# Optimization experiments

Hardware: AMD Instinct MI355X
Metric: run time of the kernel (lower is better)

Reference implementation:

```python
import jax, jax.numpy as jnp
import numpy as np

E = 1024
H = 16
F = 4096
EPS = 1e-5


def layer_norm(x, gamma, beta):
    mu = jnp.mean(x, axis=-1, keepdims=True)
    var = jnp.var(x, axis=-1, keepdims=True)
    return (x - mu) * jax.lax.rsqrt(var + EPS) * gamma + beta


def setup_inputs() -> dict:
    key = jax.random.key(0)
    ks = jax.random.split(key, 12)
    s = lambda d: 1.0 / np.sqrt(d)
    x = jax.random.normal(ks[0], (2, 2048, E), dtype=jnp.float32)
    Wq = jax.random.uniform(ks[1], (E, E), minval=-s(E), maxval=s(E))
    bq = jnp.zeros((E,), jnp.float32)
    Wk = jax.random.uniform(ks[2], (E, E), minval=-s(E), maxval=s(E))
    bk = jnp.zeros((E,), jnp.float32)
    Wv = jax.random.uniform(ks[3], (E, E), minval=-s(E), maxval=s(E))
    bv = jnp.zeros((E,), jnp.float32)
    Wo = jax.random.uniform(ks[4], (E, E), minval=-s(E), maxval=s(E))
    bo = jnp.zeros((E,), jnp.float32)
    g1 = jnp.ones((E,), jnp.float32)
    b1 = jnp.zeros((E,), jnp.float32)
    W1 = jax.random.uniform(ks[5], (E, F), minval=-s(E), maxval=s(E))
    bf1 = jnp.zeros((F,), jnp.float32)
    W2 = jax.random.uniform(ks[6], (F, E), minval=-s(F), maxval=s(F))
    bf2 = jnp.zeros((E,), jnp.float32)
    g2 = jnp.ones((E,), jnp.float32)
    b2 = jnp.zeros((E,), jnp.float32)
    return dict(x=x, Wq=Wq, bq=bq, Wk=Wk, bk=bk, Wv=Wv, bv=bv, Wo=Wo, bo=bo,
                g1=g1, b1=b1, W1=W1, bf1=bf1, W2=W2, bf2=bf2, g2=g2, b2=b2)


def reference(x, Wq, bq, Wk, bk, Wv, bv, Wo, bo, g1, b1, W1, bf1, W2, bf2, g2, b2):
    B, L, _ = x.shape
    Dh = E // H
    q = (x @ Wq + bq).reshape(B, L, H, Dh).transpose(0, 2, 1, 3)  # b h l d
    k = (x @ Wk + bk).reshape(B, L, H, Dh).transpose(0, 2, 1, 3)  # computed but unused (faithful to source)
    v = (x @ Wv + bv).reshape(B, L, H, Dh).transpose(0, 2, 1, 3)
    # NOTE: source computes scores as Q @ V^T (not K), scaled, then softmax
    scores = jnp.einsum('bhqd,bhkd->bhqk', q, v) / jnp.sqrt(jnp.float32(Dh))
    att = jax.nn.softmax(scores, axis=-1)
    ctx = jnp.einsum('bhqk,bhkd->bhqd', att, v)
    ctx = ctx.transpose(0, 2, 1, 3).reshape(B, L, E)
    att_out = ctx @ Wo + bo
    post_att = layer_norm(x + att_out, g1, b1)
    ff = jax.nn.relu(post_att @ W1 + bf1) @ W2 + bf2
    return layer_norm(post_att + ff, g2, b2)
```

## Files before the change

### kernel.cpp

```cpp
#include <hip/hip_runtime.h>
#include <stdint.h>

typedef unsigned short u16;
typedef __attribute__((ext_vector_type(8))) short short8;
typedef __attribute__((ext_vector_type(4))) float f32x4;
typedef __attribute__((ext_vector_type(4))) unsigned short u16x4;

#define TOKENS 4096
#define E_DIM 1024
#define F_DIM 4096
#define SEQ 2048
#define NH 16
#define DH 64

__device__ __forceinline__ u16 f2b(float f) {
  union { float f; unsigned u; } v; v.f = f;
  unsigned r = v.u + 0x7fffu + ((v.u >> 16) & 1u);
  return (u16)(r >> 16);
}

__device__ __forceinline__ void gl2lds16(const u16* g, u16* l) {
  __builtin_amdgcn_global_load_lds(
      (const __attribute__((address_space(1))) unsigned int*)(size_t)(g),
      (__attribute__((address_space(3))) unsigned int*)(unsigned int)(size_t)(l),
      16, 0, 0);
}

__global__ __launch_bounds__(256)
void transpose_w(const float* __restrict__ W, u16* __restrict__ Wt, int K, int N) {
  __shared__ float tile[32][33];
  const int kb = blockIdx.x * 32, nb = blockIdx.y * 32;
  const int tx = threadIdx.x & 31, ty = threadIdx.x >> 5;
#pragma unroll
  for (int i = 0; i < 32; i += 8)
    tile[ty + i][tx] = W[(size_t)(kb + ty + i) * N + nb + tx];
  __syncthreads();
#pragma unroll
  for (int i = 0; i < 32; i += 8)
    Wt[(size_t)(nb + ty + i) * K + kb + tx] = f2b(tile[tx][ty + i]);
}

__global__ __launch_bounds__(256)
void f32_to_bf16(const float* __restrict__ in, u16* __restrict__ out) {
  const int i = blockIdx.x * 256 + threadIdx.x;
  f32x4 f = ((const f32x4*)in)[i];
  u16x4 u;
#pragma unroll
  for (int j = 0; j < 4; j++) u[j] = f2b(f[j]);
  ((u16x4*)out)[i] = u;
}

__global__ __launch_bounds__(256)
void transpose_v(const u16* __restrict__ vsrc, u16* __restrict__ vt) {
  __shared__ u16 tile[32][66];
  const int kb = blockIdx.x * 32;
  const int bh = blockIdx.y;
  const int b = bh >> 4, h = bh & 15;
  {
    const int tx = threadIdx.x & 63, ty = threadIdx.x >> 6;
#pragma unroll
    for (int i = 0; i < 32; i += 4)
      tile[ty + i][tx] = vsrc[(size_t)(b * SEQ + kb + ty + i) * E_DIM + h * DH + tx];
  }
  __syncthreads();
  {
    const int kk = threadIdx.x & 31, dd = threadIdx.x >> 5;
#pragma unroll
    for (int j = 0; j < 64; j += 8)
      vt[(size_t)(bh * DH + dd + j) * SEQ + kb + kk] = tile[kk][dd + j];
  }
}

template <int RELU, int OUTBF>
__global__ __launch_bounds__(256)
void gemm_bt(const u16* __restrict__ A, const u16* __restrict__ Bt,
             const float* __restrict__ bias, void* __restrict__ Cout,
             int M, int N, int K) {
  __shared__ __align__(16) u16 As[128 * 32];
  __shared__ __align__(16) u16 Bs[128 * 32];
  const int tid = threadIdx.x;
  const int lane = tid & 63, wave = tid >> 6;
  const int mBlk = blockIdx.y * 128, nBlk = blockIdx.x * 128;
  const int wm = (wave >> 1) * 64, wn = (wave & 1) * 64;
  const int l15 = lane & 15, g = lane >> 4;

  f32x4 acc[4][4] = {};

  const int srow = lane >> 2;
  const int scol = (lane & 3) * 8;

  const u16* Ab = A + (size_t)mBlk * K;
  const u16* Bb = Bt + (size_t)nBlk * K;

  for (int k0 = 0; k0 < K; k0 += 32) {
    __syncthreads();
    for (int c = wave; c < 8; c += 4) {
      const int r = c * 16 + srow;
      gl2lds16(Ab + (size_t)r * K + k0 + scol, As + c * 512 + lane * 8);
      gl2lds16(Bb + (size_t)r * K + k0 + scol, Bs + c * 512 + lane * 8);
    }
    __syncthreads();

    short8 af[4], bf[4];
#pragma unroll
    for (int i = 0; i < 4; i++)
      af[i] = *(const short8*)(As + (wm + i * 16 + l15) * 32 + g * 8);
#pragma unroll
    for (int i = 0; i < 4; i++)
      bf[i] = *(const short8*)(Bs + (wn + i * 16 + l15) * 32 + g * 8);
#pragma unroll
    for (int mi = 0; mi < 4; mi++)
#pragma unroll
      for (int ni = 0; ni < 4; ni++)
        acc[mi][ni] = __builtin_amdgcn_mfma_f32_16x16x32_bf16(af[mi], bf[ni],
                                                              acc[mi][ni], 0, 0, 0);
  }

  const int row0 = mBlk + wm + g * 4;
  const int col0 = nBlk + wn + l15;
#pragma unroll
  for (int ni = 0; ni < 4; ni++) {
    const int c = col0 + ni * 16;
    const float bv = bias[c];
#pragma unroll
    for (int mi = 0; mi < 4; mi++) {
#pragma unroll
      for (int r = 0; r < 4; r++) {
        float v = acc[mi][ni][r] + bv;
        if (RELU) v = fmaxf(v, 0.f);
        const size_t idx = (size_t)(row0 + mi * 16 + r) * N + c;
        if (OUTBF) ((u16*)Cout)[idx] = f2b(v);
        else       ((float*)Cout)[idx] = v;
      }
    }
  }
}

template <int RELU, int OUTBF>
__global__ __launch_bounds__(256)
void gemm_bt64(const u16* __restrict__ A, const u16* __restrict__ Bt,
               const float* __restrict__ bias, void* __restrict__ Cout,
               int M, int N, int K, float oscale) {
  __shared__ __align__(16) u16 As[128 * 32];
  __shared__ __align__(16) u16 Bs[64 * 32];
  const int tid = threadIdx.x;
  const int lane = tid & 63, wave = tid >> 6;
  const int mBlk = blockIdx.y * 128, nBlk = blockIdx.x * 64;
  const int wm = (wave >> 1) * 64, wn = (wave & 1) * 32;
  const int l15 = lane & 15, g = lane >> 4;

  f32x4 acc[4][2] = {};

  const int srow = lane >> 2;
  const int scol = (lane & 3) * 8;

  const u16* Ab = A + (size_t)mBlk * K;
  const u16* Bb = Bt + (size_t)nBlk * K;

  for (int k0 = 0; k0 < K; k0 += 32) {
    __syncthreads();
    for (int c = wave; c < 8; c += 4) {
      const int r = c * 16 + srow;
      gl2lds16(Ab + (size_t)r * K + k0 + scol, As + c * 512 + lane * 8);
    }
    gl2lds16(Bb + (size_t)(wave * 16 + srow) * K + k0 + scol, Bs + wave * 512 + lane * 8);
    __syncthreads();

    short8 af[4], bf[2];
#pragma unroll
    for (int i = 0; i < 4; i++)
      af[i] = *(const short8*)(As + (wm + i * 16 + l15) * 32 + g * 8);
#pragma unroll
    for (int i = 0; i < 2; i++)
      bf[i] = *(const short8*)(Bs + (wn + i * 16 + l15) * 32 + g * 8);
#pragma unroll
    for (int mi = 0; mi < 4; mi++)
#pragma unroll
      for (int ni = 0; ni < 2; ni++)
        acc[mi][ni] = __builtin_amdgcn_mfma_f32_16x16x32_bf16(af[mi], bf[ni],
                                                              acc[mi][ni], 0, 0, 0);
  }

  const int row0 = mBlk + wm + g * 4;
  const int col0 = nBlk + wn + l15;
#pragma unroll
  for (int ni = 0; ni < 2; ni++) {
    const int c = col0 + ni * 16;
    const float bv = bias[c];
#pragma unroll
    for (int mi = 0; mi < 4; mi++) {
#pragma unroll
      for (int r = 0; r < 4; r++) {
        float v = (acc[mi][ni][r] + bv) * oscale;
        if (RELU) v = fmaxf(v, 0.f);
        const size_t idx = (size_t)(row0 + mi * 16 + r) * N + c;
        if (OUTBF) ((u16*)Cout)[idx] = f2b(v);
        else       ((float*)Cout)[idx] = v;
      }
    }
  }
}

__global__ __launch_bounds__(256)
void gemm_qv64(const u16* __restrict__ A, const u16* __restrict__ Bqv,
               const float* __restrict__ bq, const float* __restrict__ bv,
               u16* __restrict__ qout, u16* __restrict__ vout, int K) {
  __shared__ __align__(16) u16 As[128 * 32];
  __shared__ __align__(16) u16 Bs[64 * 32];
  const int tid = threadIdx.x;
  const int lane = tid & 63, wave = tid >> 6;
  const int mBlk = blockIdx.y * 128, nBlk = blockIdx.x * 64;
  const int isQ = nBlk < 1024;
  const int ncol = isQ ? nBlk : nBlk - 1024;
  const float* bias = isQ ? bq : bv;
  u16* out = isQ ? qout : vout;
  const float oscale = isQ ? 0.125f : 1.0f;
  const int wm = (wave >> 1) * 64, wn = (wave & 1) * 32;
  const int l15 = lane & 15, g = lane >> 4;

  f32x4 acc[4][2] = {};

  const int srow = lane >> 2;
  const int scol = (lane & 3) * 8;

  const u16* Ab = A + (size_t)mBlk * K;
  const u16* Bb = Bqv + (size_t)nBlk * K;

  for (int k0 = 0; k0 < K; k0 += 32) {
    __syncthreads();
    for (int c = wave; c < 8; c += 4) {
      const int r = c * 16 + srow;
      gl2lds16(Ab + (size_t)r * K + k0 + scol, As + c * 512 + lane * 8);
    }
    gl2lds16(Bb + (size_t)(wave * 16 + srow) * K + k0 + scol, Bs + wave * 512 + lane * 8);
    __syncthreads();

    short8 af[4], bf[2];
#pragma unroll
    for (int i = 0; i < 4; i++)
      af[i] = *(const short8*)(As + (wm + i * 16 + l15) * 32 + g * 8);
#pragma unroll
    for (int i = 0; i < 2; i++)
      bf[i] = *(const short8*)(Bs + (wn + i * 16 + l15) * 32 + g * 8);
#pragma unroll
    for (int mi = 0; mi < 4; mi++)
#pragma unroll
      for (int ni = 0; ni < 2; ni++)
        acc[mi][ni] = __builtin_amdgcn_mfma_f32_16x16x32_bf16(af[mi], bf[ni],
                                                              acc[mi][ni], 0, 0, 0);
  }

  const int row0 = mBlk + wm + g * 4;
  const int col0 = ncol + wn + l15;
#pragma unroll
  for (int ni = 0; ni < 2; ni++) {
    const int c = col0 + ni * 16;
    const float bv_ = bias[c];
#pragma unroll
    for (int mi = 0; mi < 4; mi++) {
#pragma unroll
      for (int r = 0; r < 4; r++) {
        float v = (acc[mi][ni][r] + bv_) * oscale;
        out[(size_t)(row0 + mi * 16 + r) * E_DIM + c] = f2b(v);
      }
    }
  }
}

__global__ __launch_bounds__(256)
void attn_kernel(const u16* __restrict__ qb, const u16* __restrict__ vb,
                 const u16* __restrict__ vtb, u16* __restrict__ ctxb) {
  __shared__ __align__(16) u16 Vs[64 * 64];
  __shared__ __align__(16) u16 Vts[64 * 64];
  __shared__ __align__(16) u16 Pl[4][16 * 64];
  const int tid = threadIdx.x;
  const int lane = tid & 63;
  const int wave = tid >> 6;
  const int l15 = lane & 15;
  const int g = lane >> 4;
  const int qblk = blockIdx.x;
  const int bh = blockIdx.y;
  const int b = bh >> 4;
  const int h = bh & 15;
  const int qrow = qblk * 64 + wave * 16;

  short8 aq0, aq1;
  {
    const u16* qp = qb + ((size_t)(b * SEQ + qrow + l15)) * E_DIM + h * DH + g * 8;
    aq0 = *(const short8*)(qp);
    aq1 = *(const short8*)(qp + 32);
  }

  f32x4 o[4] = {};
  float lsum[4] = {0.f, 0.f, 0.f, 0.f};

  const u16* vbase = vb + ((size_t)b * SEQ) * E_DIM + h * DH;
  const u16* vtbase = vtb + ((size_t)bh * DH) * SEQ;
  u16* myPl = Pl[wave];

  const int srow = tid >> 3;
  const int sch = tid & 7;

  for (int kc = 0; kc < SEQ; kc += 64) {
    __syncthreads();
#pragma unroll
    for (int j = 0; j < 2; j++) {
      const int key = j * 32 + srow;
      gl2lds16(vbase + (size_t)(kc + key) * E_DIM + ((sch ^ (key & 7)) * 8),
               Vs + key * 64 + sch * 8);
      const int d = j * 32 + srow;
      gl2lds16(vtbase + (size_t)d * SEQ + kc + ((sch ^ (d & 7)) * 8),
               Vts + d * 64 + sch * 8);
    }
    __syncthreads();

    f32x4 s[4];
#pragma unroll
    for (int nt = 0; nt < 4; nt++) {
      const int key = nt * 16 + l15;
      const u16* vr = Vs + key * 64;
      short8 b0 = *(const short8*)(vr + ((g ^ (key & 7)) * 8));
      short8 b1 = *(const short8*)(vr + (((4 + g) ^ (key & 7)) * 8));
      f32x4 z = {};
      z = __builtin_amdgcn_mfma_f32_16x16x32_bf16(aq0, b0, z, 0, 0, 0);
      z = __builtin_amdgcn_mfma_f32_16x16x32_bf16(aq1, b1, z, 0, 0, 0);
      s[nt] = z;
    }

#pragma unroll
    for (int r = 0; r < 4; r++) {
      const int q = g * 4 + r;
      u16* prow = myPl + q * 64;
#pragma unroll
      for (int nt = 0; nt < 4; nt++) {
        union { float f; unsigned u; } pv;
        pv.f = __expf(s[nt][r]);
        union { unsigned u; float f; } pt;
        pt.u = pv.u & 0xffff0000u;
        lsum[r] += pt.f;
        prow[(((nt * 2 + (l15 >> 3)) ^ (q & 7)) * 8) + (l15 & 7)] = (u16)(pt.u >> 16);
      }
    }

#pragma unroll
    for (int ks = 0; ks < 2; ks++) {
      short8 ap = *(const short8*)(myPl + l15 * 64 + (((ks * 4 + g) ^ (l15 & 7)) * 8));
#pragma unroll
      for (int dt = 0; dt < 4; dt++) {
        const int d = dt * 16 + l15;
        short8 bv = *(const short8*)(Vts + d * 64 + (((ks * 4 + g) ^ (d & 7)) * 8));
        o[dt] = __builtin_amdgcn_mfma_f32_16x16x32_bf16(ap, bv, o[dt], 0, 0, 0);
      }
    }
  }

#pragma unroll
  for (int r = 0; r < 4; r++) {
    float l = lsum[r];
    l += __shfl_xor(l, 1);
    l += __shfl_xor(l, 2);
    l += __shfl_xor(l, 4);
    l += __shfl_xor(l, 8);
    const float inv = 1.0f / l;
    size_t base = ((size_t)(b * SEQ + qrow + g * 4 + r)) * E_DIM + h * DH;
#pragma unroll
    for (int dt = 0; dt < 4; dt++)
      ctxb[base + dt * 16 + l15] = f2b(o[dt][r] * inv);
  }
}

__global__ __launch_bounds__(256)
void add_ln(const float* __restrict__ X, const float* __restrict__ Y,
            const float* __restrict__ gam, const float* __restrict__ bet,
            float* __restrict__ out32, u16* __restrict__ out16) {
  const int row = blockIdx.x;
  const int tid = threadIdx.x;
  const size_t base = (size_t)row * E_DIM;
  float v[4];
  float s = 0.f, sq = 0.f;
#pragma unroll
  for (int i = 0; i < 4; i++) {
    const int c = tid + i * 256;
    float x = X[base + c] + Y[base + c];
    v[i] = x; s += x; sq += x * x;
  }
#pragma unroll
  for (int off = 32; off; off >>= 1) {
    s += __shfl_xor(s, off);
    sq += __shfl_xor(sq, off);
  }
  __shared__ float sh[8];
  const int wave = tid >> 6, lane = tid & 63;
  if (lane == 0) { sh[wave] = s; sh[4 + wave] = sq; }
  __syncthreads();
  s = sh[0] + sh[1] + sh[2] + sh[3];
  sq = sh[4] + sh[5] + sh[6] + sh[7];
  const float mean = s * (1.f / 1024.f);
  const float var = sq * (1.f / 1024.f) - mean * mean;
  const float rstd = rsqrtf(var + 1e-5f);
#pragma unroll
  for (int i = 0; i < 4; i++) {
    const int c = tid + i * 256;
    float y = (v[i] - mean) * rstd * gam[c] + bet[c];
    out32[base + c] = y;
    if (out16) out16[base + c] = f2b(y);
  }
}

extern "C" void kernel_launch(void* const* d_in, const int* in_sizes, int n_in,
                              void* d_out, int out_size, void* d_ws, size_t ws_size,
                              hipStream_t stream) {
  const float* x   = (const float*)d_in[0];
  const float* Wq  = (const float*)d_in[1];
  const float* bq  = (const float*)d_in[2];
  const float* Wv  = (const float*)d_in[5];
  const float* bv  = (const float*)d_in[6];
  const float* Wo  = (const float*)d_in[7];
  const float* bo  = (const float*)d_in[8];
  const float* g1  = (const float*)d_in[9];
  const float* b1  = (const float*)d_in[10];
  const float* W1  = (const float*)d_in[11];
  const float* bf1 = (const float*)d_in[12];
  const float* W2  = (const float*)d_in[13];
  const float* bf2 = (const float*)d_in[14];
  const float* g2  = (const float*)d_in[15];
  const float* b2  = (const float*)d_in[16];

  char* w = (char*)d_ws;
  const size_t MB = 1024ull * 1024ull;
  u16*   xb   = (u16*)(w + 0);
  u16*   h1   = (u16*)(w + 8 * MB);
  u16*   qb   = (u16*)(w + 8 * MB);
  u16*   vb   = (u16*)(w + 16 * MB);
  u16*   vtb  = (u16*)(w + 24 * MB);
  u16*   ctxb = (u16*)(w + 32 * MB);
  float* atto = (float*)(w + 40 * MB);
  float* ff   = (float*)(w + 40 * MB);
  float* pa   = (float*)(w + 56 * MB);
  u16*   pab  = (u16*)(w + 72 * MB);
  u16*   WqT  = (u16*)(w + 80 * MB);
  u16*   WvT  = (u16*)(w + 82 * MB);
  u16*   WoT  = (u16*)(w + 84 * MB);
  u16*   W1T  = (u16*)(w + 86 * MB);
  u16*   W2T  = (u16*)(w + 94 * MB);

  transpose_w<<<dim3(32, 32), 256, 0, stream>>>(Wq, WqT, 1024, 1024);
  transpose_w<<<dim3(32, 32), 256, 0, stream>>>(Wv, WvT, 1024, 1024);
  transpose_w<<<dim3(32, 32), 256, 0, stream>>>(Wo, WoT, 1024, 1024);
  transpose_w<<<dim3(32, 128), 256, 0, stream>>>(W1, W1T, 1024, 4096);
  transpose_w<<<dim3(128, 32), 256, 0, stream>>>(W2, W2T, 4096, 1024);
  f32_to_bf16<<<TOKENS * E_DIM / 4 / 256, 256, 0, stream>>>(x, xb);

  gemm_qv64<<<dim3(32, 32), 256, 0, stream>>>(xb, WqT, bq, bv, qb, vb, 1024);
  transpose_v<<<dim3(64, 32), 256, 0, stream>>>(vb, vtb);
  attn_kernel<<<dim3(32, 32), 256, 0, stream>>>(qb, vb, vtb, ctxb);
  gemm_bt64<0, 0><<<dim3(16, 32), 256, 0, stream>>>(ctxb, WoT, bo, atto, TOKENS, 1024, 1024, 1.0f);
  add_ln<<<TOKENS, 256, 0, stream>>>(x, atto, g1, b1, pa, pab);
  gemm_bt<1, 1><<<dim3(32, 32), 256, 0, stream>>>(pab, W1T, bf1, h1, TOKENS, 4096, 1024);
  gemm_bt64<0, 0><<<dim3(16, 32), 256, 0, stream>>>(h1, W2T, bf2, ff, TOKENS, 1024, 4096, 1.0f);
  add_ln<<<TOKENS, 256, 0, stream>>>(pa, ff, g2, b2, (float*)d_out, (u16*)nullptr);
}
```

Before: 409.0 us.

## Use split-K 128x128 GEMM for N=1024 projections, reduce partials in add-LN

Replaces the 128x64-tile GEMM for the Wo and W2 projections with a 128x128-tile kernel that splits K into two halves over blockIdx.z. Each half writes its own fp32 partial buffer, with the bias added only by the first half. The layernorm kernel now sums both partials with the residual, so the reduction is fused there. The larger tile gives more data reuse per block and split-K keeps the block count at 512. The cost is extra fp32 traffic from writing and reading a second 16MB partial buffer, and the workspace layout is shifted to make room for it.

```diff
diff --git a/kernel.cpp b/kernel.cpp
--- a/kernel.cpp
+++ b/kernel.cpp
@@ -85,7 +85,6 @@
   const int l15 = lane & 15, g = lane >> 4;
 
   f32x4 acc[4][4] = {};
-
   const int srow = lane >> 2;
   const int scol = (lane & 3) * 8;
 
@@ -136,67 +135,63 @@
   }
 }
 
-template <int RELU, int OUTBF>
-__global__ __launch_bounds__(256)
-void gemm_bt64(const u16* __restrict__ A, const u16* __restrict__ Bt,
-               const float* __restrict__ bias, void* __restrict__ Cout,
-               int M, int N, int K, float oscale) {
+__global__ __launch_bounds__(256)
+void gemm_bt_sk(const u16* __restrict__ A, const u16* __restrict__ Bt,
+                const float* __restrict__ bias, float* __restrict__ Cout,
+                int M, int N, int K) {
   __shared__ __align__(16) u16 As[128 * 32];
-  __shared__ __align__(16) u16 Bs[64 * 32];
+  __shared__ __align__(16) u16 Bs[128 * 32];
   const int tid = threadIdx.x;
   const int lane = tid & 63, wave = tid >> 6;
-  const int mBlk = blockIdx.y * 128, nBlk = blockIdx.x * 64;
-  const int wm = (wave >> 1) * 64, wn = (wave & 1) * 32;
+  const int mBlk = blockIdx.y * 128, nBlk = blockIdx.x * 128;
+  const int kz = blockIdx.z;
+  const int Kh = K >> 1;
+  const int wm = (wave >> 1) * 64, wn = (wave & 1) * 64;
   const int l15 = lane & 15, g = lane >> 4;
 
-  f32x4 acc[4][2] = {};
-
+  f32x4 acc[4][4] = {};
   const int srow = lane >> 2;
   const int scol = (lane & 3) * 8;
 
-  const u16* Ab = A + (size_t)mBlk * K;
-  const u16* Bb = Bt + (size_t)nBlk * K;
-
-  for (int k0 = 0; k0 < K; k0 += 32) {
+  const u16* Ab = A + (size_t)mBlk * K + (size_t)kz * Kh;
+  const u16* Bb = Bt + (size_t)nBlk * K + (size_t)kz * Kh;
+
+  for (int k0 = 0; k0 < Kh; k0 += 32) {
     __syncthreads();
     for (int c = wave; c < 8; c += 4) {
       const int r = c * 16 + srow;
       gl2lds16(Ab + (size_t)r * K + k0 + scol, As + c * 512 + lane * 8);
-    }
-    gl2lds16(Bb + (size_t)(wave * 16 + srow) * K + k0 + scol, Bs + wave * 512 + lane * 8);
-    __syncthreads();
-
-    short8 af[4], bf[2];
+      gl2lds16(Bb + (size_t)r * K + k0 + scol, Bs + c * 512 + lane * 8);
+    }
+    __syncthreads();
+
+    short8 af[4], bf[4];
 #pragma unroll
     for (int i = 0; i < 4; i++)
       af[i] = *(const short8*)(As + (wm + i * 16 + l15) * 32 + g * 8);
 #pragma unroll
-    for (int i = 0; i < 2; i++)
+    for (int i = 0; i < 4; i++)
       bf[i] = *(const short8*)(Bs + (wn + i * 16 + l15) * 32 + g * 8);
 #pragma unroll
     for (int mi = 0; mi < 4; mi++)
 #pragma unroll
-      for (int ni = 0; ni < 2; ni++)
+      for (int ni = 0; ni < 4; ni++)
         acc[mi][ni] = __builtin_amdgcn_mfma_f32_16x16x32_bf16(af[mi], bf[ni],
                                                               acc[mi][ni], 0, 0, 0);
   }
 
+  float* out = Cout + (size_t)kz * M * N;
   const int row0 = mBlk + wm + g * 4;
   const int col0 = nBlk + wn + l15;
 #pragma unroll
-  for (int ni = 0; ni < 2; ni++) {
+  for (int ni = 0; ni < 4; ni++) {
     const int c = col0 + ni * 16;
-    const float bv = bias[c];
+    const float bv = (kz == 0) ? bias[c] : 0.f;
 #pragma unroll
     for (int mi = 0; mi < 4; mi++) {
 #pragma unroll
-      for (int r = 0; r < 4; r++) {
-        float v = (acc[mi][ni][r] + bv) * oscale;
-        if (RELU) v = fmaxf(v, 0.f);
-        const size_t idx = (size_t)(row0 + mi * 16 + r) * N + c;
-        if (OUTBF) ((u16*)Cout)[idx] = f2b(v);
-        else       ((float*)Cout)[idx] = v;
-      }
+      for (int r = 0; r < 4; r++)
+        out[(size_t)(row0 + mi * 16 + r) * N + c] = acc[mi][ni][r] + bv;
     }
   }
 }
@@ -219,7 +214,6 @@
   const int l15 = lane & 15, g = lane >> 4;
 
   f32x4 acc[4][2] = {};
-
   const int srow = lane >> 2;
   const int scol = (lane & 3) * 8;
 
@@ -370,9 +364,10 @@
 }
 
 __global__ __launch_bounds__(256)
-void add_ln(const float* __restrict__ X, const float* __restrict__ Y,
-            const float* __restrict__ gam, const float* __restrict__ bet,
-            float* __restrict__ out32, u16* __restrict__ out16) {
+void add_ln3(const float* __restrict__ X, const float* __restrict__ Y0,
+             const float* __restrict__ Y1,
+             const float* __restrict__ gam, const float* __restrict__ bet,
+             float* __restrict__ out32, u16* __restrict__ out16) {
   const int row = blockIdx.x;
   const int tid = threadIdx.x;
   const size_t base = (size_t)row * E_DIM;
@@ -381,7 +376,7 @@
 #pragma unroll
   for (int i = 0; i < 4; i++) {
     const int c = tid + i * 256;
-    float x = X[base + c] + Y[base + c];
+    float x = X[base + c] + Y0[base + c] + Y1[base + c];
     v[i] = x; s += x; sq += x * x;
   }
 #pragma unroll
@@ -434,15 +429,15 @@
   u16*   vb   = (u16*)(w + 16 * MB);
   u16*   vtb  = (u16*)(w + 24 * MB);
   u16*   ctxb = (u16*)(w + 32 * MB);
-  float* atto = (float*)(w + 40 * MB);
-  float* ff   = (float*)(w + 40 * MB);
-  float* pa   = (float*)(w + 56 * MB);
-  u16*   pab  = (u16*)(w + 72 * MB);
-  u16*   WqT  = (u16*)(w + 80 * MB);
-  u16*   WvT  = (u16*)(w + 82 * MB);
-  u16*   WoT  = (u16*)(w + 84 * MB);
-  u16*   W1T  = (u16*)(w + 86 * MB);
-  u16*   W2T  = (u16*)(w + 94 * MB);
+  float* att0 = (float*)(w + 40 * MB);
+  float* ff0  = (float*)(w + 40 * MB);
+  float* pa   = (float*)(w + 72 * MB);
+  u16*   pab  = (u16*)(w + 88 * MB);
+  u16*   WqT  = (u16*)(w + 96 * MB);
+  u16*   WvT  = (u16*)(w + 98 * MB);
+  u16*   WoT  = (u16*)(w + 100 * MB);
+  u16*   W1T  = (u16*)(w + 102 * MB);
+  u16*   W2T  = (u16*)(w + 110 * MB);
 
   transpose_w<<<dim3(32, 32), 256, 0, stream>>>(Wq, WqT, 1024, 1024);
   transpose_w<<<dim3(32, 32), 256, 0, stream>>>(Wv, WvT, 1024, 1024);
@@ -454,9 +449,9 @@
   gemm_qv64<<<dim3(32, 32), 256, 0, stream>>>(xb, WqT, bq, bv, qb, vb, 1024);
   transpose_v<<<dim3(64, 32), 256, 0, stream>>>(vb, vtb);
   attn_kernel<<<dim3(32, 32), 256, 0, stream>>>(qb, vb, vtb, ctxb);
-  gemm_bt64<0, 0><<<dim3(16, 32), 256, 0, stream>>>(ctxb, WoT, bo, atto, TOKENS, 1024, 1024, 1.0f);
-  add_ln<<<TOKENS, 256, 0, stream>>>(x, atto, g1, b1, pa, pab);
+  gemm_bt_sk<<<dim3(8, 32, 2), 256, 0, stream>>>(ctxb, WoT, bo, att0, TOKENS, 1024, 1024);
+  add_ln3<<<TOKENS, 256, 0, stream>>>(x, att0, att0 + (size_t)TOKENS * 1024, g1, b1, pa, pab);
   gemm_bt<1, 1><<<dim3(32, 32), 256, 0, stream>>>(pab, W1T, bf1, h1, TOKENS, 4096, 1024);
-  gemm_bt64<0, 0><<<dim3(16, 32), 256, 0, stream>>>(h1, W2T, bf2, ff, TOKENS, 1024, 4096, 1.0f);
-  add_ln<<<TOKENS, 256, 0, stream>>>(pa, ff, g2, b2, (float*)d_out, (u16*)nullptr);
-}
+  gemm_bt_sk<<<dim3(8, 32, 2), 256, 0, stream>>>(h1, W2T, bf2, ff0, TOKENS, 1024, 4096);
+  add_ln3<<<TOKENS, 256, 0, stream>>>(pa, ff0, ff0 + (size_t)TOKENS * 1024, g2, b2, (float*)d_out, (u16*)nullptr);
+}
```

Result: faster. 392.7 us (-4.0%).
